# Kernel tuning notes

Measured on AMD Instinct MI355X. Metric: run time of the kernel, lower is better.

Reference implementation:

```python
import jax, jax.numpy as jnp
import numpy as np

BETA = 0.95
THRESHOLD = 1.0  # snntorch Leaky default
DELAY = 5
CHOSEN_W1 = 0.5
UTE = 1.01
T, B = 50, 500000


def setup_inputs() -> dict:
    key = jax.random.key(0)
    k1, _ = jax.random.split(key)
    spike_seq = (jax.random.uniform(k1, (T, B, 2), dtype=jnp.float32) < 0.05).astype(jnp.float32)
    w1 = float(CHOSEN_W1)
    w2 = float(UTE) - float(BETA) ** int(DELAY) * w1
    W = jnp.array([[w1, w2]], dtype=jnp.float32)  # fc.weight, shape [1, 2]
    return {"spike_seq": spike_seq, "W": W}


def _spike(x):
    # Heaviside fire function (snntorch fire): spk = 1[x > 0]
    return (x > 0).astype(x.dtype)


def reference(spike_seq, W):
    # snntorch Leaky (reset-by-subtraction, applied from previous step's spike):
    #   reset_t = 1[mem_{t-1} - thr > 0]
    #   mem_t   = beta * mem_{t-1} + cur_t - reset_t * thr
    #   spk_t   = 1[mem_t - thr > 0]
    cur_seq = jnp.einsum('tbi,oi->tbo', spike_seq, W)  # [T, B, 1]

    def step(mem, cur):
        reset = _spike(mem - THRESHOLD)
        mem_new = BETA * mem + cur - reset * THRESHOLD
        spk = _spike(mem_new - THRESHOLD)
        return mem_new, spk

    mem0 = jnp.zeros((spike_seq.shape[1], 1), dtype=spike_seq.dtype)
    _, spk_rec = jax.lax.scan(step, mem0, cur_seq)
    return spk_rec  # [T, B, 1]
```

## Files before the change

kernel.cpp:

```cpp
#include <hip/hip_runtime.h>


constexpr int T_STEPS = 50;
constexpr int BATCH   = 500000;
constexpr int HALF    = BATCH / 2;

__global__ __launch_bounds__(256)
void snn_leaky_kernel(const float4* __restrict__ in4,
                      const float*  __restrict__ W,
                      float2*       __restrict__ out2)
{
    const int i = blockIdx.x * blockDim.x + threadIdx.x;
    if (i >= HALF) return;

    const float w1 = W[0];
    const float w2 = W[1];

    float mem0 = 0.0f, mem1 = 0.0f;

    const float4* __restrict__ p = in4 + i;
    float2*       __restrict__ q = out2 + i;

    #pragma unroll 5
    for (int t = 0; t < T_STEPS; ++t) {
        const float4 s = p[(size_t)t * HALF];

        const float cur0 = __fadd_rn(__fmul_rn(s.x, w1), __fmul_rn(s.y, w2));
        const float cur1 = __fadd_rn(__fmul_rn(s.z, w1), __fmul_rn(s.w, w2));

        const float r0 = (mem0 > 1.0f) ? 1.0f : 0.0f;
        const float r1 = (mem1 > 1.0f) ? 1.0f : 0.0f;

        mem0 = __fsub_rn(__fadd_rn(__fmul_rn(0.95f, mem0), cur0), r0);
        mem1 = __fsub_rn(__fadd_rn(__fmul_rn(0.95f, mem1), cur1), r1);

        float2 spk;
        spk.x = (mem0 > 1.0f) ? 1.0f : 0.0f;
        spk.y = (mem1 > 1.0f) ? 1.0f : 0.0f;
        q[(size_t)t * HALF] = spk;
    }
}

extern "C" void kernel_launch(void* const* d_in, const int* in_sizes, int n_in,
                              void* d_out, int out_size, void* d_ws, size_t ws_size,
                              hipStream_t stream) {
    const float4* in4 = (const float4*)d_in[0];
    const float*  W   = (const float*)d_in[1];
    float2*       out = (float2*)d_out;

    const int threads = 256;
    const int blocks  = (HALF + threads - 1) / threads;
    snn_leaky_kernel<<<blocks, threads, 0, stream>>>(in4, W, out);
}
```

Measured before the change: 302.3 us.

## Process four neurons per thread with register prefetch and nontemporal accesses

```diff
diff --git a/kernel.cpp b/kernel.cpp
--- a/kernel.cpp
+++ b/kernel.cpp
@@ -3,52 +3,77 @@
 
 constexpr int T_STEPS = 50;
 constexpr int BATCH   = 500000;
-constexpr int HALF    = BATCH / 2;
+constexpr int QUART   = BATCH / 4;
+constexpr int PF      = 5;
+
+typedef float v4f __attribute__((ext_vector_type(4)));
 
 __global__ __launch_bounds__(256)
-void snn_leaky_kernel(const float4* __restrict__ in4,
-                      const float*  __restrict__ W,
-                      float2*       __restrict__ out2)
+void snn_leaky_kernel(const v4f* __restrict__ in4,
+                      const float* __restrict__ W,
+                      v4f*        __restrict__ out4)
 {
     const int i = blockIdx.x * blockDim.x + threadIdx.x;
-    if (i >= HALF) return;
+    if (i >= QUART) return;
 
     const float w1 = W[0];
     const float w2 = W[1];
 
-    float mem0 = 0.0f, mem1 = 0.0f;
+    float m0 = 0.0f, m1 = 0.0f, m2 = 0.0f, m3 = 0.0f;
 
-    const float4* __restrict__ p = in4 + i;
-    float2*       __restrict__ q = out2 + i;
+    const v4f* __restrict__ p = in4 + (size_t)2 * i;
+    v4f*       __restrict__ q = out4 + i;
 
-    #pragma unroll 5
+    v4f bufA[PF], bufB[PF];
+    #pragma unroll
+    for (int k = 0; k < PF; ++k) {
+        const v4f* r = p + (size_t)k * (BATCH / 2);
+        bufA[k] = __builtin_nontemporal_load(r);
+        bufB[k] = __builtin_nontemporal_load(r + 1);
+    }
+
+    #pragma unroll
     for (int t = 0; t < T_STEPS; ++t) {
-        const float4 s = p[(size_t)t * HALF];
+        const v4f sA = bufA[t % PF];
+        const v4f sB = bufB[t % PF];
+        if (t + PF < T_STEPS) {
+            const v4f* r = p + (size_t)(t + PF) * (BATCH / 2);
+            bufA[t % PF] = __builtin_nontemporal_load(r);
+            bufB[t % PF] = __builtin_nontemporal_load(r + 1);
+        }
 
-        const float cur0 = __fadd_rn(__fmul_rn(s.x, w1), __fmul_rn(s.y, w2));
-        const float cur1 = __fadd_rn(__fmul_rn(s.z, w1), __fmul_rn(s.w, w2));
+        const float c0 = __fadd_rn(__fmul_rn(sA.x, w1), __fmul_rn(sA.y, w2));
+        const float c1 = __fadd_rn(__fmul_rn(sA.z, w1), __fmul_rn(sA.w, w2));
+        const float c2 = __fadd_rn(__fmul_rn(sB.x, w1), __fmul_rn(sB.y, w2));
+        const float c3 = __fadd_rn(__fmul_rn(sB.z, w1), __fmul_rn(sB.w, w2));
 
-        const float r0 = (mem0 > 1.0f) ? 1.0f : 0.0f;
-        const float r1 = (mem1 > 1.0f) ? 1.0f : 0.0f;
+        const float r0 = (m0 > 1.0f) ? 1.0f : 0.0f;
+        const float r1 = (m1 > 1.0f) ? 1.0f : 0.0f;
+        const float r2 = (m2 > 1.0f) ? 1.0f : 0.0f;
+        const float r3 = (m3 > 1.0f) ? 1.0f : 0.0f;
 
-        mem0 = __fsub_rn(__fadd_rn(__fmul_rn(0.95f, mem0), cur0), r0);
-        mem1 = __fsub_rn(__fadd_rn(__fmul_rn(0.95f, mem1), cur1), r1);
+        m0 = __fsub_rn(__fadd_rn(__fmul_rn(0.95f, m0), c0), r0);
+        m1 = __fsub_rn(__fadd_rn(__fmul_rn(0.95f, m1), c1), r1);
+        m2 = __fsub_rn(__fadd_rn(__fmul_rn(0.95f, m2), c2), r2);
+        m3 = __fsub_rn(__fadd_rn(__fmul_rn(0.95f, m3), c3), r3);
 
-        float2 spk;
-        spk.x = (mem0 > 1.0f) ? 1.0f : 0.0f;
-        spk.y = (mem1 > 1.0f) ? 1.0f : 0.0f;
-        q[(size_t)t * HALF] = spk;
+        v4f spk;
+        spk.x = (m0 > 1.0f) ? 1.0f : 0.0f;
+        spk.y = (m1 > 1.0f) ? 1.0f : 0.0f;
+        spk.z = (m2 > 1.0f) ? 1.0f : 0.0f;
+        spk.w = (m3 > 1.0f) ? 1.0f : 0.0f;
+        __builtin_nontemporal_store(spk, &q[(size_t)t * QUART]);
     }
 }
 
 extern "C" void kernel_launch(void* const* d_in, const int* in_sizes, int n_in,
                               void* d_out, int out_size, void* d_ws, size_t ws_size,
                               hipStream_t stream) {
-    const float4* in4 = (const float4*)d_in[0];
-    const float*  W   = (const float*)d_in[1];
-    float2*       out = (float2*)d_out;
+    const v4f*   in4 = (const v4f*)d_in[0];
+    const float* W   = (const float*)d_in[1];
+    v4f*         out = (v4f*)d_out;
 
     const int threads = 256;
-    const int blocks  = (HALF + threads - 1) / threads;
+    const int blocks  = (QUART + threads - 1) / threads;
     snn_leaky_kernel<<<blocks, threads, 0, stream>>>(in4, W, out);
 }
```

Measured after the change: 289.7 us. 1.04x faster.
